# Kernel tuning notes

Measured on AMD Instinct MI355X. Metric: run time of the kernel, lower is better.

The kernel has to match this reference:

```python
import jax, jax.numpy as jnp
import numpy as np

COMMITMENT_COST = 1.0


def setup_inputs() -> dict:
    key = jax.random.key(0)
    k1, k2 = jax.random.split(key)
    x = jax.random.normal(k1, (8, 4096, 256), dtype=jnp.float32)
    codebook = jax.random.normal(k2, (2048, 256), dtype=jnp.float32)
    return {"x": x, "codebook": codebook}


def reference(x, codebook):
    # Squared Euclidean distances via the GEMM expansion:
    # argmin over torch.cdist (sqrt is monotone); dist values are unused.
    x2 = jnp.sum(x * x, axis=-1, keepdims=True)            # [B, T, 1]
    c2 = jnp.sum(codebook * codebook, axis=-1)             # [N]
    d2 = x2 - 2.0 * jnp.einsum('btd,nd->btn', x, codebook) + c2  # [B, T, N]
    indices = jnp.argmin(d2, axis=-1)                      # [B, T]
    codes = codebook[indices]                              # [B, T, D]

    code_loss = jnp.mean((codes - jax.lax.stop_gradient(x)) ** 2)
    embedding_loss = jnp.mean((x - jax.lax.stop_gradient(codes)) ** 2) * COMMITMENT_COST
    loss = code_loss + embedding_loss

    # Straight-through estimator
    quantized = x + jax.lax.stop_gradient(codes - x)
    return quantized, indices, loss
```

## Files before the change

### kernel.cpp

```cpp
#include <hip/hip_runtime.h>

#define D   256
#define BM  64
#define BN  128

typedef __attribute__((ext_vector_type(8))) short v8s;
typedef __attribute__((ext_vector_type(4))) float v4f;
#define MFMA16 __builtin_amdgcn_mfma_f32_16x16x32_bf16

#define WAITVM(N) asm volatile("s_waitcnt vmcnt(" #N ")" ::: "memory")
#define SCHEDFENCE() __builtin_amdgcn_sched_barrier(0)

static __device__ inline unsigned short f2bf(float f) {
    unsigned u = __float_as_uint(f);
    return (unsigned short)((u + 0x7fffu + ((u >> 16) & 1u)) >> 16);
}
static __device__ inline float bf2f(unsigned short s) {
    return __uint_as_float(((unsigned)s) << 16);
}

static __device__ inline void gl_lds16(const unsigned short* g, unsigned short* l) {
    __builtin_amdgcn_global_load_lds(
        (const __attribute__((address_space(1))) unsigned int*)g,
        (__attribute__((address_space(3))) unsigned int*)l, 16, 0, 0);
}

__global__ void vq_prep_c2(const float* __restrict__ cb, float* __restrict__ c2,
                           float* __restrict__ loss) {
    const int row  = blockIdx.x;
    const int lane = threadIdx.x;
    if (row == 0 && lane == 0) loss[0] = 0.0f;
    const float4 v = *reinterpret_cast<const float4*>(cb + (size_t)row * D + lane * 4);
    float s = v.x * v.x + v.y * v.y + v.z * v.z + v.w * v.w;
    #pragma unroll
    for (int off = 32; off > 0; off >>= 1) s += __shfl_down(s, off, 64);
    if (lane == 0) c2[row] = s;
}

__global__ void vq_prep_sw(const float* __restrict__ cb,
                           unsigned short* __restrict__ cbh, unsigned short* __restrict__ cbl) {
    const int b     = blockIdx.x;
    const int chunk = b >> 2;
    const int nc = (chunk >> 2) * BN;
    const int kc = (chunk & 3) * 64;
    const int p   = (b & 3) * 256 + threadIdx.x;
    const int seg = p >> 7;
    const int n   = (p & 127) ^ seg;
    const float* src = cb + (size_t)(nc + n) * D + kc + seg * 8;
    const float4 f0 = *reinterpret_cast<const float4*>(src);
    const float4 f1 = *reinterpret_cast<const float4*>(src + 4);
    const float f[8] = {f0.x, f0.y, f0.z, f0.w, f1.x, f1.y, f1.z, f1.w};
    v8s h, l;
    #pragma unroll
    for (int j = 0; j < 8; ++j) {
        unsigned short hb = f2bf(f[j]);
        h[j] = (short)hb;
        l[j] = (short)f2bf(f[j] - bf2f(hb));
    }
    const size_t o = ((size_t)chunk * 1024 + p) * 8;
    *reinterpret_cast<v8s*>(cbh + o) = h;
    *reinterpret_cast<v8s*>(cbl + o) = l;
}

__global__ __launch_bounds__(256, 2) void vq_argmin_mfma(
        const float* __restrict__ x, const float* __restrict__ cb,
        const unsigned short* __restrict__ cbh, const unsigned short* __restrict__ cbl,
        const float* __restrict__ c2, float* __restrict__ idx_out,
        float* __restrict__ qout, float* __restrict__ loss, float scale, int N) {
    __shared__ unsigned short lds_h[2][8192];
    __shared__ unsigned short lds_l[2][8192];
    __shared__ float c2s[2048];

    const int tid  = threadIdx.x;
    const int w    = tid >> 6;
    const int lane = tid & 63;
    const int col  = lane & 15;
    const int quad = lane >> 4;
    const int mg   = w >> 1;
    const int ng   = w & 1;
    const int m0   = blockIdx.x * BM;
    const int n_groups = N >> 7;
    const int n_stages = n_groups * 4;

    const unsigned short* gh0 = cbh + ((size_t)(w * 256 + lane)) * 8;
    const unsigned short* gl0 = cbl + ((size_t)(w * 256 + lane)) * 8;

    #pragma unroll
    for (int i = 0; i < 4; ++i) {
        gl_lds16(gh0 + i * 512, &lds_h[0][(w * 256 + i * 64) * 8]);
        gl_lds16(gl0 + i * 512, &lds_l[0][(w * 256 + i * 64) * 8]);
    }

    {
        const int o = tid * 8;
        if (o < N) {
            const float4 a = *reinterpret_cast<const float4*>(c2 + o);
            const float4 b = *reinterpret_cast<const float4*>(c2 + o + 4);
            *reinterpret_cast<float4*>(&c2s[o])     = a;
            *reinterpret_cast<float4*>(&c2s[o + 4]) = b;
        }
    }

    v8s xh[2][8], xl[2][8];
    #pragma unroll
    for (int mt = 0; mt < 2; ++mt) {
        const float* xr = x + (size_t)(m0 + mg * 32 + mt * 16 + col) * D;
        #pragma unroll
        for (int ks = 0; ks < 8; ++ks) {
            const int kb = ks * 32 + quad * 8;
            const float4 f0 = *reinterpret_cast<const float4*>(xr + kb);
            const float4 f1 = *reinterpret_cast<const float4*>(xr + kb + 4);
            float f[8] = {f0.x, f0.y, f0.z, f0.w, f1.x, f1.y, f1.z, f1.w};
            v8s h, l;
            #pragma unroll
            for (int j = 0; j < 8; ++j) {
                unsigned short hb = f2bf(f[j]);
                h[j] = (short)hb;
                l[j] = (short)f2bf(f[j] - bf2f(hb));
            }
            xh[mt][ks] = h; xl[mt][ks] = l;
        }
    }

    float runmin[2][4];
    int   runidx[2][4];
    #pragma unroll
    for (int mt = 0; mt < 2; ++mt)
        #pragma unroll
        for (int r = 0; r < 4; ++r) { runmin[mt][r] = 3.4e38f; runidx[mt][r] = 0; }

    v4f acc[4][2];
    #pragma unroll
    for (int nt = 0; nt < 4; ++nt)
        #pragma unroll
        for (int mt = 0; mt < 2; ++mt) acc[nt][mt] = 0.0f;

    __syncthreads();

    for (int g = 0; g < n_groups; ++g) {
        #pragma unroll
        for (int cc = 0; cc < 4; ++cc) {
            const int par   = cc & 1;
            const int stage = g * 4 + cc;
            const bool more = (stage + 1 < n_stages);

            SCHEDFENCE();
            WAITVM(0);
            SCHEDFENCE();
            __builtin_amdgcn_s_barrier();
            SCHEDFENCE();
            if (more) {
                const unsigned short* gh = gh0 + (size_t)(stage + 1) * 8192;
                const unsigned short* gl = gl0 + (size_t)(stage + 1) * 8192;
                unsigned short* lh = &lds_h[par ^ 1][0];
                unsigned short* ll = &lds_l[par ^ 1][0];
                #pragma unroll
                for (int i = 0; i < 4; ++i) {
                    gl_lds16(gh + i * 512, lh + (w * 256 + i * 64) * 8);
                    gl_lds16(gl + i * 512, ll + (w * 256 + i * 64) * 8);
                }
            }
            __builtin_amdgcn_s_setprio(1);
            #pragma unroll
            for (int ksk = 0; ksk < 2; ++ksk) {
                const int ks  = cc * 2 + ksk;
                const int seg = ksk * 4 + quad;
                #pragma unroll
                for (int nt = 0; nt < 4; ++nt) {
                    const int p = seg * BN + ((ng * 64 + nt * 16 + col) ^ seg);
                    const v8s ch = *reinterpret_cast<const v8s*>(&lds_h[par][p * 8]);
                    const v8s cl = *reinterpret_cast<const v8s*>(&lds_l[par][p * 8]);
                    #pragma unroll
                    for (int mt = 0; mt < 2; ++mt) {
                        acc[nt][mt] = MFMA16(xh[mt][ks], ch, acc[nt][mt], 0, 0, 0);
                        acc[nt][mt] = MFMA16(xl[mt][ks], ch, acc[nt][mt], 0, 0, 0);
                        acc[nt][mt] = MFMA16(xh[mt][ks], cl, acc[nt][mt], 0, 0, 0);
                    }
                }
            }
            __builtin_amdgcn_s_setprio(0);
        }

        #pragma unroll
        for (int nt = 0; nt < 4; ++nt) {
            const int n = g * BN + ng * 64 + nt * 16 + col;
            const float c2n = c2s[n];
            #pragma unroll
            for (int mt = 0; mt < 2; ++mt) {
                #pragma unroll
                for (int r = 0; r < 4; ++r) {
                    const float s = c2n - 2.0f * acc[nt][mt][r];
                    if (s < runmin[mt][r]) { runmin[mt][r] = s; runidx[mt][r] = n; }
                }
                acc[nt][mt] = 0.0f;
            }
        }
    }

    __syncthreads();
    float* red_v = reinterpret_cast<float*>(&lds_h[0][0]);
    int*   red_i = reinterpret_cast<int*>(&lds_l[0][0]);
    #pragma unroll
    for (int mt = 0; mt < 2; ++mt)
        #pragma unroll
        for (int r = 0; r < 4; ++r) {
            const int row  = mg * 32 + mt * 16 + quad * 4 + r;
            const int slot = (ng * 16 + col) ^ (row & 31);
            red_v[row * 32 + slot] = runmin[mt][r];
            red_i[row * 32 + slot] = runidx[mt][r];
        }
    __syncthreads();
    float best = 3.4e38f;
    int   bidx = 0;
    if (tid < 64) {
        #pragma unroll 4
        for (int t = 0; t < 32; ++t) {
            const int  sl = t ^ (tid & 31);
            const float v = red_v[tid * 32 + sl];
            const int  id = red_i[tid * 32 + sl];
            if (v < best || (v == best && id < bidx)) { best = v; bidx = id; }
        }
        idx_out[m0 + tid] = (float)bidx;
    }
    __syncthreads();
    int* idx_sh = reinterpret_cast<int*>(&lds_h[1][0]);
    if (tid < 64) idx_sh[tid] = bidx;
    __syncthreads();

    const float* xg2 = x + (size_t)m0 * D;
    float s = 0.0f;
    #pragma unroll
    for (int i = 0; i < 16; ++i) {
        const int gix = i * 256 + tid;
        const int row = gix >> 6;
        const int k4  = (gix & 63) * 4;
        const int idx = idx_sh[row];
        const float4 c  = *reinterpret_cast<const float4*>(cb  + (size_t)idx * D + k4);
        const float4 xv = *reinterpret_cast<const float4*>(xg2 + (size_t)row * D + k4);
        *reinterpret_cast<float4*>(qout + (size_t)(m0 + row) * D + k4) = c;
        const float dx = c.x - xv.x, dy = c.y - xv.y, dz = c.z - xv.z, dw = c.w - xv.w;
        s += dx * dx + dy * dy + dz * dz + dw * dw;
    }
    #pragma unroll
    for (int off = 32; off > 0; off >>= 1) s += __shfl_down(s, off, 64);
    float* wsum = reinterpret_cast<float*>(&lds_l[1][0]);
    if ((tid & 63) == 0) wsum[tid >> 6] = s;
    __syncthreads();
    if (tid == 0) {
        atomicAdd(loss, (wsum[0] + wsum[1] + wsum[2] + wsum[3]) * scale);
    }
}

extern "C" void kernel_launch(void* const* d_in, const int* in_sizes, int n_in,
                              void* d_out, int out_size, void* d_ws, size_t ws_size,
                              hipStream_t stream) {
    const float* x  = (const float*)d_in[0];
    const float* cb = (const float*)d_in[1];
    const int M = in_sizes[0] / D;
    const int N = in_sizes[1] / D;

    float* qout    = (float*)d_out;
    float* idx_out = qout + (size_t)M * D;
    float* loss    = idx_out + M;

    char* wsb = (char*)d_ws;
    float*          c2  = (float*)wsb;
    unsigned short* cbh = (unsigned short*)(wsb + 8192);
    unsigned short* cbl = cbh + (size_t)N * D;

    vq_prep_c2<<<N, 64, 0, stream>>>(cb, c2, loss);
    vq_prep_sw<<<(N / BN) * 4 * 4, 256, 0, stream>>>(cb, cbh, cbl);
    const float scale = 2.0f / (float)((size_t)M * D);
    vq_argmin_mfma<<<M / BM, 256, 0, stream>>>(x, cb, cbh, cbl, c2, idx_out, qout,
                                               loss, scale, N);
}
```

Measured before the change: 194.5 us.

## Load codebook MFMA fragments directly from global into registers, bypassing LDS

The prep kernel now writes the bf16 hi/lo codebook in exact per-lane MFMA fragment order. The main kernel drops the LDS double buffer and its per-stage barriers, and instead has each wave load its B fragments straight from global into double-buffered registers. Launch bounds drop to one block per CU so the larger register footprint fits. The trade-off is duplicated global/L2 traffic, since both M-group waves fetch the same fragments, along with lower occupancy to hide global latency. The final prefetch also reads one stage past the end of the hi array.

```diff
diff --git a/kernel.cpp b/kernel.cpp
--- a/kernel.cpp
+++ b/kernel.cpp
@@ -7,9 +7,7 @@
 typedef __attribute__((ext_vector_type(8))) short v8s;
 typedef __attribute__((ext_vector_type(4))) float v4f;
 #define MFMA16 __builtin_amdgcn_mfma_f32_16x16x32_bf16
-
-#define WAITVM(N) asm volatile("s_waitcnt vmcnt(" #N ")" ::: "memory")
-#define SCHEDFENCE() __builtin_amdgcn_sched_barrier(0)
+#define SB0() __builtin_amdgcn_sched_barrier(0)
 
 static __device__ inline unsigned short f2bf(float f) {
     unsigned u = __float_as_uint(f);
@@ -17,12 +15,6 @@
 }
 static __device__ inline float bf2f(unsigned short s) {
     return __uint_as_float(((unsigned)s) << 16);
-}
-
-static __device__ inline void gl_lds16(const unsigned short* g, unsigned short* l) {
-    __builtin_amdgcn_global_load_lds(
-        (const __attribute__((address_space(1))) unsigned int*)g,
-        (__attribute__((address_space(3))) unsigned int*)l, 16, 0, 0);
 }
 
 __global__ void vq_prep_c2(const float* __restrict__ cb, float* __restrict__ c2,
@@ -37,39 +29,45 @@
     if (lane == 0) c2[row] = s;
 }
 
-__global__ void vq_prep_sw(const float* __restrict__ cb,
-                           unsigned short* __restrict__ cbh, unsigned short* __restrict__ cbl) {
-    const int b     = blockIdx.x;
-    const int chunk = b >> 2;
-    const int nc = (chunk >> 2) * BN;
-    const int kc = (chunk & 3) * 64;
-    const int p   = (b & 3) * 256 + threadIdx.x;
-    const int seg = p >> 7;
-    const int n   = (p & 127) ^ seg;
-    const float* src = cb + (size_t)(nc + n) * D + kc + seg * 8;
+__global__ void vq_prep_frag(const float* __restrict__ cb,
+                             unsigned short* __restrict__ cbh,
+                             unsigned short* __restrict__ cbl) {
+    const int p   = blockIdx.x * 256 + threadIdx.x;
+    const int col = p & 15;
+    const int q   = (p >> 4) & 3;
+    const int f   = (p >> 6) & 7;
+    const int ng  = (p >> 9) & 1;
+    const int s   = p >> 10;
+    const int g = s >> 2, cc = s & 3;
+    const int nt = f & 3, ksk = f >> 2;
+    const int seg = ksk * 4 + q;
+    const int n  = g * 128 + ng * 64 + nt * 16 + col;
+    const int k0 = cc * 64 + seg * 8;
+    const float* src = cb + (size_t)n * D + k0;
     const float4 f0 = *reinterpret_cast<const float4*>(src);
     const float4 f1 = *reinterpret_cast<const float4*>(src + 4);
-    const float f[8] = {f0.x, f0.y, f0.z, f0.w, f1.x, f1.y, f1.z, f1.w};
+    const float fv[8] = {f0.x, f0.y, f0.z, f0.w, f1.x, f1.y, f1.z, f1.w};
     v8s h, l;
     #pragma unroll
     for (int j = 0; j < 8; ++j) {
-        unsigned short hb = f2bf(f[j]);
+        unsigned short hb = f2bf(fv[j]);
         h[j] = (short)hb;
-        l[j] = (short)f2bf(f[j] - bf2f(hb));
-    }
-    const size_t o = ((size_t)chunk * 1024 + p) * 8;
-    *reinterpret_cast<v8s*>(cbh + o) = h;
-    *reinterpret_cast<v8s*>(cbl + o) = l;
-}
-
-__global__ __launch_bounds__(256, 2) void vq_argmin_mfma(
+        l[j] = (short)f2bf(fv[j] - bf2f(hb));
+    }
+    *reinterpret_cast<v8s*>(cbh + (size_t)p * 8) = h;
+    *reinterpret_cast<v8s*>(cbl + (size_t)p * 8) = l;
+}
+
+__global__ __launch_bounds__(256, 1) void vq_argmin_mfma(
         const float* __restrict__ x, const float* __restrict__ cb,
         const unsigned short* __restrict__ cbh, const unsigned short* __restrict__ cbl,
         const float* __restrict__ c2, float* __restrict__ idx_out,
         float* __restrict__ qout, float* __restrict__ loss, float scale, int N) {
-    __shared__ unsigned short lds_h[2][8192];
-    __shared__ unsigned short lds_l[2][8192];
+    __shared__ float red_v[64 * 32];
+    __shared__ int   red_i[64 * 32];
     __shared__ float c2s[2048];
+    __shared__ int   idx_sh[64];
+    __shared__ float wsum[4];
 
     const int tid  = threadIdx.x;
     const int w    = tid >> 6;
@@ -80,16 +78,23 @@
     const int ng   = w & 1;
     const int m0   = blockIdx.x * BM;
     const int n_groups = N >> 7;
-    const int n_stages = n_groups * 4;
-
-    const unsigned short* gh0 = cbh + ((size_t)(w * 256 + lane)) * 8;
-    const unsigned short* gl0 = cbl + ((size_t)(w * 256 + lane)) * 8;
-
-    #pragma unroll
-    for (int i = 0; i < 4; ++i) {
-        gl_lds16(gh0 + i * 512, &lds_h[0][(w * 256 + i * 64) * 8]);
-        gl_lds16(gl0 + i * 512, &lds_l[0][(w * 256 + i * 64) * 8]);
-    }
+
+    const char* bh = (const char*)cbh + (size_t)ng * 8192 + (size_t)lane * 16;
+    const char* bl = (const char*)cbl + (size_t)ng * 8192 + (size_t)lane * 16;
+
+#define LOADB(CH, CL, S)                                                       \
+    {                                                                          \
+        const char* ph = bh + (size_t)(S) * 16384;                             \
+        const char* pl = bl + (size_t)(S) * 16384;                             \
+        _Pragma("unroll")                                                      \
+        for (int f = 0; f < 8; ++f) {                                          \
+            CH[f] = *reinterpret_cast<const v8s*>(ph + f * 1024);              \
+            CL[f] = *reinterpret_cast<const v8s*>(pl + f * 1024);              \
+        }                                                                      \
+    }
+
+    v8s chA[8], clA[8], chB[8], clB[8];
+    LOADB(chA, clA, 0);
 
     {
         const int o = tid * 8;
@@ -110,13 +115,13 @@
             const int kb = ks * 32 + quad * 8;
             const float4 f0 = *reinterpret_cast<const float4*>(xr + kb);
             const float4 f1 = *reinterpret_cast<const float4*>(xr + kb + 4);
-            float f[8] = {f0.x, f0.y, f0.z, f0.w, f1.x, f1.y, f1.z, f1.w};
+            float fv[8] = {f0.x, f0.y, f0.z, f0.w, f1.x, f1.y, f1.z, f1.w};
             v8s h, l;
             #pragma unroll
             for (int j = 0; j < 8; ++j) {
-                unsigned short hb = f2bf(f[j]);
+                unsigned short hb = f2bf(fv[j]);
                 h[j] = (short)hb;
-                l[j] = (short)f2bf(f[j] - bf2f(hb));
+                l[j] = (short)f2bf(fv[j] - bf2f(hb));
             }
             xh[mt][ks] = h; xl[mt][ks] = l;
         }
@@ -137,49 +142,33 @@
 
     __syncthreads();
 
+#define COMP(CH, CL, CC)                                                       \
+    _Pragma("unroll")                                                          \
+    for (int ksk = 0; ksk < 2; ++ksk) {                                        \
+        const int ks = (CC) * 2 + ksk;                                         \
+        _Pragma("unroll")                                                      \
+        for (int nt = 0; nt < 4; ++nt) {                                       \
+            const v8s ch = CH[ksk * 4 + nt];                                   \
+            const v8s cl = CL[ksk * 4 + nt];                                   \
+            _Pragma("unroll")                                                  \
+            for (int mt = 0; mt < 2; ++mt) {                                   \
+                acc[nt][mt] = MFMA16(xh[mt][ks], ch, acc[nt][mt], 0, 0, 0);    \
+                acc[nt][mt] = MFMA16(xl[mt][ks], ch, acc[nt][mt], 0, 0, 0);    \
+                acc[nt][mt] = MFMA16(xh[mt][ks], cl, acc[nt][mt], 0, 0, 0);    \
+            }                                                                  \
+        }                                                                      \
+    }
+
     for (int g = 0; g < n_groups; ++g) {
-        #pragma unroll
-        for (int cc = 0; cc < 4; ++cc) {
-            const int par   = cc & 1;
-            const int stage = g * 4 + cc;
-            const bool more = (stage + 1 < n_stages);
-
-            SCHEDFENCE();
-            WAITVM(0);
-            SCHEDFENCE();
-            __builtin_amdgcn_s_barrier();
-            SCHEDFENCE();
-            if (more) {
-                const unsigned short* gh = gh0 + (size_t)(stage + 1) * 8192;
-                const unsigned short* gl = gl0 + (size_t)(stage + 1) * 8192;
-                unsigned short* lh = &lds_h[par ^ 1][0];
-                unsigned short* ll = &lds_l[par ^ 1][0];
-                #pragma unroll
-                for (int i = 0; i < 4; ++i) {
-                    gl_lds16(gh + i * 512, lh + (w * 256 + i * 64) * 8);
-                    gl_lds16(gl + i * 512, ll + (w * 256 + i * 64) * 8);
-                }
-            }
-            __builtin_amdgcn_s_setprio(1);
-            #pragma unroll
-            for (int ksk = 0; ksk < 2; ++ksk) {
-                const int ks  = cc * 2 + ksk;
-                const int seg = ksk * 4 + quad;
-                #pragma unroll
-                for (int nt = 0; nt < 4; ++nt) {
-                    const int p = seg * BN + ((ng * 64 + nt * 16 + col) ^ seg);
-                    const v8s ch = *reinterpret_cast<const v8s*>(&lds_h[par][p * 8]);
-                    const v8s cl = *reinterpret_cast<const v8s*>(&lds_l[par][p * 8]);
-                    #pragma unroll
-                    for (int mt = 0; mt < 2; ++mt) {
-                        acc[nt][mt] = MFMA16(xh[mt][ks], ch, acc[nt][mt], 0, 0, 0);
-                        acc[nt][mt] = MFMA16(xl[mt][ks], ch, acc[nt][mt], 0, 0, 0);
-                        acc[nt][mt] = MFMA16(xh[mt][ks], cl, acc[nt][mt], 0, 0, 0);
-                    }
-                }
-            }
-            __builtin_amdgcn_s_setprio(0);
-        }
+        const int s0 = g * 4;
+        LOADB(chB, clB, s0 + 1); SB0();
+        COMP(chA, clA, 0);
+        LOADB(chA, clA, s0 + 2); SB0();
+        COMP(chB, clB, 1);
+        LOADB(chB, clB, s0 + 3); SB0();
+        COMP(chA, clA, 2);
+        LOADB(chA, clA, s0 + 4); SB0();
+        COMP(chB, clB, 3);
 
         #pragma unroll
         for (int nt = 0; nt < 4; ++nt) {
@@ -196,10 +185,10 @@
             }
         }
     }
-
-    __syncthreads();
-    float* red_v = reinterpret_cast<float*>(&lds_h[0][0]);
-    int*   red_i = reinterpret_cast<int*>(&lds_l[0][0]);
+#undef LOADB
+#undef COMP
+
+    __syncthreads();
     #pragma unroll
     for (int mt = 0; mt < 2; ++mt)
         #pragma unroll
@@ -221,10 +210,8 @@
             if (v < best || (v == best && id < bidx)) { best = v; bidx = id; }
         }
         idx_out[m0 + tid] = (float)bidx;
-    }
-    __syncthreads();
-    int* idx_sh = reinterpret_cast<int*>(&lds_h[1][0]);
-    if (tid < 64) idx_sh[tid] = bidx;
+        idx_sh[tid] = bidx;
+    }
     __syncthreads();
 
     const float* xg2 = x + (size_t)m0 * D;
@@ -243,7 +230,6 @@
     }
     #pragma unroll
     for (int off = 32; off > 0; off >>= 1) s += __shfl_down(s, off, 64);
-    float* wsum = reinterpret_cast<float*>(&lds_l[1][0]);
     if ((tid & 63) == 0) wsum[tid >> 6] = s;
     __syncthreads();
     if (tid == 0) {
@@ -269,7 +255,7 @@
     unsigned short* cbl = cbh + (size_t)N * D;
 
     vq_prep_c2<<<N, 64, 0, stream>>>(cb, c2, loss);
-    vq_prep_sw<<<(N / BN) * 4 * 4, 256, 0, stream>>>(cb, cbh, cbl);
+    vq_prep_frag<<<(N * D * 2 / 16) / 256, 256, 0, stream>>>(cb, cbh, cbl);
     const float scale = 2.0f / (float)((size_t)M * D);
     vq_argmin_mfma<<<M / BM, 256, 0, stream>>>(x, cb, cbh, cbl, c2, idx_out, qout,
                                                loss, scale, N);
```

After: 181.6 us. 6.6% less time.
